# Kernel tuning notes

Measured on AMD Instinct MI355X. Metric: run time of the kernel, lower is better.

Reference implementation:

```python
import jax, jax.numpy as jnp
import numpy as np

N_NODES = 100000
N_EDGES = 3200000
IN_C, HID_C, OUT_C = 64, 128, 64


def gcn_conv(x, src, dst, W, b, n):
    """PyG GCNConv: h = x @ W; out[d] += norm(e) * h[s]; norm = deg^-1/2[s]*deg^-1/2[d].
    src/dst already include self-loops."""
    h = x @ W  # [N, out_c]
    deg = jax.ops.segment_sum(jnp.ones_like(dst, dtype=h.dtype), dst, num_segments=n)
    dinv = jnp.where(deg > 0, jax.lax.rsqrt(deg), 0.0)
    norm = dinv[src] * dinv[dst]  # [E]
    msg = h[src] * norm[:, None]  # [E, out_c] -- dominant memory traffic
    return jax.ops.segment_sum(msg, dst, num_segments=n) + b


def setup_inputs() -> dict:
    key = jax.random.key(0)
    k1, k2, k3, k4 = jax.random.split(key, 4)
    x = jax.random.normal(k1, (N_NODES, IN_C), dtype=jnp.float32)
    edge_index = jax.random.randint(k2, (2, N_EDGES), 0, N_NODES, dtype=jnp.int64)
    W1 = jax.random.normal(k3, (IN_C, HID_C), dtype=jnp.float32) / np.sqrt(IN_C)
    b1 = jnp.zeros((HID_C,), dtype=jnp.float32)
    W2 = jax.random.normal(k4, (HID_C, OUT_C), dtype=jnp.float32) / np.sqrt(HID_C)
    b2 = jnp.zeros((OUT_C,), dtype=jnp.float32)
    return {"x": x, "edge_index": edge_index, "W1": W1, "b1": b1, "W2": W2, "b2": b2}


def reference(x, edge_index, W1, b1, W2, b2):
    n = x.shape[0]
    loops = jnp.arange(n, dtype=edge_index.dtype)  # self-loops, as PyG GCNConv adds
    src = jnp.concatenate([edge_index[0], loops])
    dst = jnp.concatenate([edge_index[1], loops])
    h = gcn_conv(x, src, dst, W1, b1, n)
    h = jax.nn.relu(h)
    out = gcn_conv(h, src, dst, W2, b2, n)
    return out
```

## Files before the change

kernel.cpp:

```cpp
#include <hip/hip_runtime.h>
#include <math.h>


#define IN_C 64
#define HID_C 128
#define OUT_C 64
#define BSHIFT 9
#define BW (1 << BSHIFT)
#define NPB 512
#define CAP 24576
#define CH_MAX 6272

typedef __attribute__((ext_vector_type(8))) short bf16x8;
typedef __attribute__((ext_vector_type(4))) float f32x4;
typedef __attribute__((ext_vector_type(2))) float v2f;

__device__ __forceinline__ unsigned short f2bf(float f) {
  unsigned u = __float_as_uint(f);
  return (unsigned short)((u + 0x7FFF + ((u >> 16) & 1)) >> 16);
}
__device__ __forceinline__ v2f cvt2(unsigned u) {
  v2f r;
  r.x = __uint_as_float(u << 16);
  r.y = __uint_as_float(u & 0xFFFF0000u);
  return r;
}
__device__ __forceinline__ unsigned pack2(v2f v) {
  return ((unsigned)f2bf(v.y) << 16) | f2bf(v.x);
}


__global__ __launch_bounds__(256) void k_build(const int* __restrict__ ei, int e, int n,
    int nb, int* __restrict__ gcnt, unsigned* __restrict__ ebuf,
    const float* __restrict__ W1, const float* __restrict__ W2,
    unsigned short* __restrict__ Wt1, unsigned short* __restrict__ Wt2,
    unsigned short* __restrict__ xs_zero, unsigned short* __restrict__ h2s_zero) {
  const int t = threadIdx.x;
  if (blockIdx.x >= NPB) {
    int bb = blockIdx.x - NPB;
    if (bb == 32) {
      if (t < 64) { xs_zero[t] = 0; h2s_zero[t] = 0; }
      return;
    }
    int i = bb * 256 + t;
    if (i < IN_C * HID_C) {
      int k = i >> 7, c = i & (HID_C - 1);
      Wt1[c * IN_C + k] = f2bf(W1[i]);
    }
    if (i < HID_C * OUT_C) {
      int k = i >> 6, c = i & (OUT_C - 1);
      Wt2[c * HID_C + k] = f2bf(W2[i]);
    }
    return;
  }
  __shared__ unsigned lpay[CH_MAX];
  __shared__ unsigned char lbuck[CH_MAX];
  __shared__ int lh[256];
  __shared__ int lbase[256];
  __shared__ int lcur[256];
  __shared__ int sflag;
  if (t == 0) sflag = 0;
  __syncthreads();
  const int chunk = (e + NPB - 1) / NPB;
  const int lo = blockIdx.x * chunk;
  const int hi = min(lo + chunk, e);
  {
    int lim = min(hi, lo + 512);
    int f = 0;
    for (int i = lo + t; i < lim; i += 256)
      if (ei[2 * i + 1] != 0) f = 1;
    if (f) sflag = 1;
  }
  __syncthreads();
  const int f = sflag;
  for (int sub = lo; sub < hi; sub += CH_MAX) {
    const int shi = min(sub + CH_MAX, hi);
    const int mm = shi - sub;
    for (int i = t; i < nb; i += 256) lh[i] = 0;
    __syncthreads();
    for (int i = sub + t; i < shi; i += 256) {
      int s, d;
      if (f) {
        s = __builtin_nontemporal_load(&ei[i]);
        d = __builtin_nontemporal_load(&ei[e + i]);
      } else {
        s = (int)__builtin_nontemporal_load(&((const long long*)ei)[i]);
        d = (int)__builtin_nontemporal_load(&((const long long*)ei)[e + i]);
      }
      s = min(max(s, 0), n - 1);
      d = min(max(d, 0), n - 1);
      int bk = d >> BSHIFT;
      lpay[i - sub] = ((unsigned)(d & (BW - 1)) << 23) | (unsigned)s;
      lbuck[i - sub] = (unsigned char)bk;
      atomicAdd(&lh[bk], 1);
    }
    __syncthreads();
    for (int i = t; i < nb; i += 256) {
      int c = lh[i];
      lbase[i] = c ? atomicAdd(&gcnt[i], c) : 0;
      lcur[i] = 0;
    }
    __syncthreads();
    for (int i = t; i < mm; i += 256) {
      int bk = lbuck[i];
      int slot = lbase[bk] + atomicAdd(&lcur[bk], 1);
      if (slot < CAP) ebuf[(size_t)bk * CAP + slot] = lpay[i];
    }
    __syncthreads();
  }
}


__global__ __launch_bounds__(1024) void k_finalize(const unsigned* __restrict__ ebuf,
    const int* __restrict__ gcnt, const float* __restrict__ x,
    unsigned short* __restrict__ xs, int n, int nb,
    int* __restrict__ row_ptr, float* __restrict__ dinv, int* __restrict__ col) {
  __shared__ int sc[256];
  __shared__ int ldeg[BW];
  __shared__ int lofs[BW];
  __shared__ int lcur[BW];
  __shared__ float sdv[BW];
  __shared__ int wsum[256];
  const int b = blockIdx.x;
  const int t = threadIdx.x;
  const int T = 1024;
  int cnt = 0, nodes = 0;
  if (t < nb) {
    cnt = min(gcnt[t], CAP);
    nodes = min(BW, n - t * BW);
  }
  if (t < 256) sc[t] = cnt + nodes;
  __syncthreads();
  for (int off = 1; off < 256; off <<= 1) {
    int vc = 0;
    if (t < 256 && t >= off) vc = sc[t - off];
    __syncthreads();
    if (t < 256) sc[t] += vc;
    __syncthreads();
  }
  const int cntb = min(gcnt[b], CAP);
  const int eb = b * CAP;
  const int ee = eb + cntb;
  const int cb = (b == 0) ? 0 : sc[b - 1];
  const int lo = b * BW;
  const int nn = min(BW, n - lo);
  for (int k = t; k < BW; k += T) ldeg[k] = 0;
  __syncthreads();
  for (int k = t; k < nn; k += T) ldeg[k] = 1;
  __syncthreads();
  for (int j = eb + t; j < ee; j += T) {
    int dl = (int)(ebuf[j] >> 23);
    atomicAdd(&ldeg[dl], 1);
  }
  __syncthreads();
  int p0 = 0, p1 = 0;
  if (t < 256) {
    p0 = ldeg[2 * t]; p1 = ldeg[2 * t + 1];
    wsum[t] = p0 + p1;
  }
  __syncthreads();
  for (int off = 1; off < 256; off <<= 1) {
    int v = 0;
    if (t < 256 && t >= off) v = wsum[t - off];
    __syncthreads();
    if (t < 256) wsum[t] += v;
    __syncthreads();
  }
  if (t < 256) {
    int pb = (t == 0) ? 0 : wsum[t - 1];
    lofs[2 * t] = pb;
    lofs[2 * t + 1] = pb + p0;
  }
  __syncthreads();
  for (int k = t; k < nn; k += T) {
    int base = cb + lofs[k];
    float dv = rsqrtf((float)ldeg[k]);
    row_ptr[lo + k] = base;
    dinv[lo + k] = dv;
    sdv[k] = dv;
    col[base] = lo + k;
    lcur[k] = lofs[k] + 1;
  }
  if (b == nb - 1 && t == 0) row_ptr[n] = sc[nb - 1];
  __syncthreads();
  for (int j = eb + t; j < ee; j += T) {
    unsigned pk = ebuf[j];
    int s = (int)(pk & 0x7FFFFF);
    int dl = (int)(pk >> 23);
    int p = atomicAdd(&lcur[dl], 1);
    col[cb + p] = s;
  }
  const float4* x4 = (const float4*)x;
  for (int idx = t; idx < nn * 16; idx += T) {
    int row = idx >> 4, q = idx & 15;
    float sc2 = sdv[row];
    float4 v = x4[(size_t)(lo + row) * 16 + q];
    ushort4 o;
    o.x = f2bf(v.x * sc2); o.y = f2bf(v.y * sc2);
    o.z = f2bf(v.z * sc2); o.w = f2bf(v.w * sc2);
    ((ushort4*)xs)[(size_t)(lo + row) * 16 + q] = o;
  }
}


template<bool BIAS, bool OUT_BF16>
__global__ __launch_bounds__(256) void k_agg(const unsigned short* __restrict__ feat,
    const int* __restrict__ row_ptr, const int* __restrict__ col,
    const float* __restrict__ dinv, const float* __restrict__ bias,
    void* __restrict__ outv, int n) {
  const int wid = threadIdx.x >> 6;
  const int lane = threadIdx.x & 63;
  const int es = lane >> 3;
  const int c8 = lane & 7;
  const int d = blockIdx.x * 4 + wid;
  if (d >= n) return;
  const int beg = row_ptr[d], end = row_ptr[d + 1];
  const uint4* f16 = (const uint4*)feat;
  const int rem = end - beg - es;
  const int c = (rem > 0) ? ((rem + 7) >> 3) : 0;
  const int last = end - 1;
  v2f a0 = {0.f, 0.f}, a1 = {0.f, 0.f}, a2 = {0.f, 0.f}, a3 = {0.f, 0.f};
  for (int g = 0; g < c; g += 4) {
    int j0 = beg + es + 8 * g;
    int i0 = col[j0];
    int i1 = col[min(j0 + 8, last)];
    int i2 = col[min(j0 + 16, last)];
    int i3 = col[min(j0 + 24, last)];
    if (g + 1 >= c) i1 = n;
    if (g + 2 >= c) i2 = n;
    if (g + 3 >= c) i3 = n;
    uint4 u0 = f16[(size_t)i0 * 8 + c8];
    uint4 u1 = f16[(size_t)i1 * 8 + c8];
    uint4 u2 = f16[(size_t)i2 * 8 + c8];
    uint4 u3 = f16[(size_t)i3 * 8 + c8];
    a0 += cvt2(u0.x) + cvt2(u1.x) + cvt2(u2.x) + cvt2(u3.x);
    a1 += cvt2(u0.y) + cvt2(u1.y) + cvt2(u2.y) + cvt2(u3.y);
    a2 += cvt2(u0.z) + cvt2(u1.z) + cvt2(u2.z) + cvt2(u3.z);
    a3 += cvt2(u0.w) + cvt2(u1.w) + cvt2(u2.w) + cvt2(u3.w);
  }
#pragma unroll
  for (int off = 8; off <= 32; off <<= 1) {
    v2f o0, o1, o2, o3;
    o0.x = __shfl_xor(a0.x, off); o0.y = __shfl_xor(a0.y, off);
    o1.x = __shfl_xor(a1.x, off); o1.y = __shfl_xor(a1.y, off);
    o2.x = __shfl_xor(a2.x, off); o2.y = __shfl_xor(a2.y, off);
    o3.x = __shfl_xor(a3.x, off); o3.y = __shfl_xor(a3.y, off);
    a0 += o0; a1 += o1; a2 += o2; a3 += o3;
  }
  if (es == 0) {
    float sc = dinv[d];
    v2f vs = {sc, sc};
    a0 *= vs; a1 *= vs; a2 *= vs; a3 *= vs;
    if (BIAS) {
      const v2f* b2v = (const v2f*)bias;
      a0 += b2v[c8 * 4 + 0]; a1 += b2v[c8 * 4 + 1];
      a2 += b2v[c8 * 4 + 2]; a3 += b2v[c8 * 4 + 3];
    }
    if (OUT_BF16) {
      uint4 o;
      o.x = pack2(a0); o.y = pack2(a1); o.z = pack2(a2); o.w = pack2(a3);
      ((uint4*)outv)[(size_t)d * 8 + c8] = o;
    } else {
      float4* o4 = (float4*)outv;
      o4[(size_t)d * 16 + c8 * 2]     = make_float4(a0.x, a0.y, a1.x, a1.y);
      o4[(size_t)d * 16 + c8 * 2 + 1] = make_float4(a2.x, a2.y, a3.x, a3.y);
    }
  }
}


__global__ __launch_bounds__(256) void k_mlp(const unsigned short* __restrict__ A1,
    const unsigned short* __restrict__ Wt1, const unsigned short* __restrict__ Wt2,
    const float* __restrict__ b1, const float* __restrict__ dinv,
    unsigned short* __restrict__ h2s, int M) {
  __shared__ unsigned short sA[16 * 136];
  const int wv = threadIdx.x >> 6;
  const int lane = threadIdx.x & 63;
  const int m = lane & 15;
  const int q = lane >> 4;
  bf16x8 w1a[2], w1b[2], w2[4];
#pragma unroll
  for (int kt = 0; kt < 2; kt++) {
    w1a[kt] = *(const bf16x8*)&Wt1[(size_t)(wv * 16 + m) * IN_C + kt * 32 + q * 8];
    w1b[kt] = *(const bf16x8*)&Wt1[(size_t)((wv + 4) * 16 + m) * IN_C + kt * 32 + q * 8];
  }
#pragma unroll
  for (int kt = 0; kt < 4; kt++)
    w2[kt] = *(const bf16x8*)&Wt2[(size_t)(wv * 16 + m) * HID_C + kt * 32 + q * 8];
  const float bv0 = b1[wv * 16 + m];
  const float bv1 = b1[(wv + 4) * 16 + m];
  const int ntiles = (M + 15) >> 4;
  for (int tile = blockIdx.x; tile < ntiles; tile += gridDim.x) {
    const int r0 = tile * 16;
    const int ra = min(r0 + m, M - 1);
    f32x4 acc0 = {0.f, 0.f, 0.f, 0.f}, acc1 = {0.f, 0.f, 0.f, 0.f};
#pragma unroll
    for (int kt = 0; kt < 2; kt++) {
      bf16x8 a = *(const bf16x8*)&A1[(size_t)ra * IN_C + kt * 32 + q * 8];
      acc0 = __builtin_amdgcn_mfma_f32_16x16x32_bf16(a, w1a[kt], acc0, 0, 0, 0);
      acc1 = __builtin_amdgcn_mfma_f32_16x16x32_bf16(a, w1b[kt], acc1, 0, 0, 0);
    }
    float dv[4];
#pragma unroll
    for (int i = 0; i < 4; i++) dv[i] = dinv[min(r0 + q * 4 + i, M - 1)];
    {
      int c = wv * 16 + m;
#pragma unroll
      for (int i = 0; i < 4; i++)
        sA[(q * 4 + i) * 136 + c] = f2bf(fmaxf(acc0[i] + bv0, 0.f) * dv[i]);
      c = (wv + 4) * 16 + m;
#pragma unroll
      for (int i = 0; i < 4; i++)
        sA[(q * 4 + i) * 136 + c] = f2bf(fmaxf(acc1[i] + bv1, 0.f) * dv[i]);
    }
    __syncthreads();
    f32x4 acc = {0.f, 0.f, 0.f, 0.f};
#pragma unroll
    for (int kt = 0; kt < 4; kt++) {
      bf16x8 a = *(const bf16x8*)&sA[m * 136 + kt * 32 + q * 8];
      acc = __builtin_amdgcn_mfma_f32_16x16x32_bf16(a, w2[kt], acc, 0, 0, 0);
    }
    int c = wv * 16 + m;
#pragma unroll
    for (int i = 0; i < 4; i++) {
      int row = r0 + q * 4 + i;
      if (row < M) h2s[(size_t)row * OUT_C + c] = f2bf(acc[i]);
    }
    __syncthreads();
  }
}


extern "C" void kernel_launch(void* const* d_in, const int* in_sizes, int n_in,
                              void* d_out, int out_size, void* d_ws, size_t ws_size,
                              hipStream_t stream) {
  const float* x  = (const float*)d_in[0];
  const int*   ei = (const int*)d_in[1];
  const float* W1 = (const float*)d_in[2];
  const float* b1 = (const float*)d_in[3];
  const float* W2 = (const float*)d_in[4];
  const float* b2 = (const float*)d_in[5];
  float* out = (float*)d_out;

  const int n = in_sizes[0] / IN_C;
  const int e = in_sizes[1] / 2;
  const int nb = (n + BW - 1) >> BSHIFT;

  char* p = (char*)d_ws;
  auto alloc = [&](size_t bytes) {
    char* r = p;
    p += (bytes + 255) & ~(size_t)255;
    return r;
  };
  int*   gcnt       = (int*)alloc((size_t)nb * 4);
  int*   row_ptr    = (int*)alloc((size_t)(n + 1) * 4);
  float* dinv       = (float*)alloc((size_t)n * 4);
  int*   col        = (int*)alloc((size_t)(e + n) * 4);
  unsigned* ebuf    = (unsigned*)alloc((size_t)nb * CAP * 4);
  unsigned short* xs  = (unsigned short*)alloc((size_t)(n + 1) * IN_C * 2);
  unsigned short* A1  = (unsigned short*)alloc((size_t)n * IN_C * 2);
  unsigned short* h2s = (unsigned short*)alloc((size_t)(n + 1) * OUT_C * 2);
  unsigned short* Wt1 = (unsigned short*)alloc((size_t)IN_C * HID_C * 2);
  unsigned short* Wt2 = (unsigned short*)alloc((size_t)HID_C * OUT_C * 2);

  hipMemsetAsync(gcnt, 0, (size_t)nb * 4, stream);

  k_build<<<NPB + 33, 256, 0, stream>>>(ei, e, n, nb, gcnt, ebuf, W1, W2, Wt1, Wt2,
      xs + (size_t)n * IN_C, h2s + (size_t)n * OUT_C);
  k_finalize<<<nb, 1024, 0, stream>>>(ebuf, gcnt, x, xs, n, nb, row_ptr, dinv, col);

  k_agg<false, true><<<(n + 3) / 4, 256, 0, stream>>>(xs, row_ptr, col, dinv, nullptr, A1, n);
  k_mlp<<<1024, 256, 0, stream>>>(A1, Wt1, Wt2, b1, dinv, h2s, n);
  k_agg<true, false><<<(n + 3) / 4, 256, 0, stream>>>(h2s, row_ptr, col, dinv, b2, out, n);
}
```

Baseline: 279.6 us.

## Store layer-1 features column-chunked so each aggregation block gathers one 16-byte slice

Changes the scaled bf16 input features and the first aggregation output to a chunk-major layout of 8 column groups of 8 bf16 each. The first-layer aggregation becomes a new kernel in which each block handles one column group, with each wave covering 8 destination rows and 8 edge lanes per row. This is meant to shrink the gathered working set per pass, so each 1.6 MB slice fits in cache and random gathers hit L2 more often. In exchange the edge list and index reads are repeated 8 times, and the MLP reads A1 with a strided chunk-major access.

```diff
diff --git a/kernel.cpp b/kernel.cpp
--- a/kernel.cpp
+++ b/kernel.cpp
@@ -34,12 +34,16 @@
     int nb, int* __restrict__ gcnt, unsigned* __restrict__ ebuf,
     const float* __restrict__ W1, const float* __restrict__ W2,
     unsigned short* __restrict__ Wt1, unsigned short* __restrict__ Wt2,
-    unsigned short* __restrict__ xs_zero, unsigned short* __restrict__ h2s_zero) {
+    unsigned short* __restrict__ xs_cm, unsigned short* __restrict__ h2s_zero) {
   const int t = threadIdx.x;
   if (blockIdx.x >= NPB) {
     int bb = blockIdx.x - NPB;
     if (bb == 32) {
-      if (t < 64) { xs_zero[t] = 0; h2s_zero[t] = 0; }
+      if (t < 64) {
+        int c = t >> 3, k = t & 7;
+        xs_cm[((size_t)c * (n + 1) + n) * 8 + k] = 0;
+        h2s_zero[t] = 0;
+      }
       return;
     }
     int i = bb * 256 + t;
@@ -113,7 +117,7 @@
 
 __global__ __launch_bounds__(1024) void k_finalize(const unsigned* __restrict__ ebuf,
     const int* __restrict__ gcnt, const float* __restrict__ x,
-    unsigned short* __restrict__ xs, int n, int nb,
+    unsigned short* __restrict__ xs_cm, int n, int nb,
     int* __restrict__ row_ptr, float* __restrict__ dinv, int* __restrict__ col) {
   __shared__ int sc[256];
   __shared__ int ldeg[BW];
@@ -191,23 +195,83 @@
     col[cb + p] = s;
   }
   const float4* x4 = (const float4*)x;
-  for (int idx = t; idx < nn * 16; idx += T) {
-    int row = idx >> 4, q = idx & 15;
-    float sc2 = sdv[row];
-    float4 v = x4[(size_t)(lo + row) * 16 + q];
-    ushort4 o;
-    o.x = f2bf(v.x * sc2); o.y = f2bf(v.y * sc2);
-    o.z = f2bf(v.z * sc2); o.w = f2bf(v.w * sc2);
-    ((ushort4*)xs)[(size_t)(lo + row) * 16 + q] = o;
-  }
-}
-
-
-template<bool BIAS, bool OUT_BF16>
-__global__ __launch_bounds__(256) void k_agg(const unsigned short* __restrict__ feat,
+  uint4* xso = (uint4*)xs_cm;
+  for (int idx = t; idx < 8 * 512; idx += T) {
+    int c = idx >> 9, row = idx & 511;
+    if (row < nn) {
+      float sc2 = sdv[row];
+      float4 v0 = x4[(size_t)(lo + row) * 16 + c * 2];
+      float4 v1 = x4[(size_t)(lo + row) * 16 + c * 2 + 1];
+      uint4 o;
+      o.x = pack2(v2f{v0.x * sc2, v0.y * sc2});
+      o.y = pack2(v2f{v0.z * sc2, v0.w * sc2});
+      o.z = pack2(v2f{v1.x * sc2, v1.y * sc2});
+      o.w = pack2(v2f{v1.z * sc2, v1.w * sc2});
+      xso[(size_t)c * (n + 1) + lo + row] = o;
+    }
+  }
+}
+
+
+__global__ __launch_bounds__(256) void k_agg1c(const unsigned short* __restrict__ xs_cm,
+    const int* __restrict__ row_ptr, const int* __restrict__ col,
+    const float* __restrict__ dinv, unsigned short* __restrict__ A1_cm, int n) {
+  const int g = blockIdx.x & 7;
+  const int tile = blockIdx.x >> 3;
+  const int wv = threadIdx.x >> 6;
+  const int lane = threadIdx.x & 63;
+  const int rloc = lane >> 3;
+  const int es = lane & 7;
+  const int d = tile * 32 + wv * 8 + rloc;
+  if (d >= n) return;
+  const uint4* f = (const uint4*)xs_cm + (size_t)g * (n + 1);
+  const int beg = row_ptr[d], end = row_ptr[d + 1];
+  const int rem = end - beg - es;
+  const int c = (rem > 0) ? ((rem + 7) >> 3) : 0;
+  const int last = end - 1;
+  v2f a0 = {0.f, 0.f}, a1 = {0.f, 0.f}, a2 = {0.f, 0.f}, a3 = {0.f, 0.f};
+  for (int gi = 0; gi < c; gi += 4) {
+    int j0 = beg + es + 8 * gi;
+    int i0 = col[j0];
+    int i1 = col[min(j0 + 8, last)];
+    int i2 = col[min(j0 + 16, last)];
+    int i3 = col[min(j0 + 24, last)];
+    if (gi + 1 >= c) i1 = n;
+    if (gi + 2 >= c) i2 = n;
+    if (gi + 3 >= c) i3 = n;
+    uint4 u0 = f[i0];
+    uint4 u1 = f[i1];
+    uint4 u2 = f[i2];
+    uint4 u3 = f[i3];
+    a0 += cvt2(u0.x) + cvt2(u1.x) + cvt2(u2.x) + cvt2(u3.x);
+    a1 += cvt2(u0.y) + cvt2(u1.y) + cvt2(u2.y) + cvt2(u3.y);
+    a2 += cvt2(u0.z) + cvt2(u1.z) + cvt2(u2.z) + cvt2(u3.z);
+    a3 += cvt2(u0.w) + cvt2(u1.w) + cvt2(u2.w) + cvt2(u3.w);
+  }
+#pragma unroll
+  for (int off = 1; off <= 4; off <<= 1) {
+    v2f o0, o1, o2, o3;
+    o0.x = __shfl_xor(a0.x, off); o0.y = __shfl_xor(a0.y, off);
+    o1.x = __shfl_xor(a1.x, off); o1.y = __shfl_xor(a1.y, off);
+    o2.x = __shfl_xor(a2.x, off); o2.y = __shfl_xor(a2.y, off);
+    o3.x = __shfl_xor(a3.x, off); o3.y = __shfl_xor(a3.y, off);
+    a0 += o0; a1 += o1; a2 += o2; a3 += o3;
+  }
+  if (es == 0) {
+    float sc = dinv[d];
+    v2f vs = {sc, sc};
+    a0 *= vs; a1 *= vs; a2 *= vs; a3 *= vs;
+    uint4 o;
+    o.x = pack2(a0); o.y = pack2(a1); o.z = pack2(a2); o.w = pack2(a3);
+    ((uint4*)A1_cm)[(size_t)g * n + d] = o;
+  }
+}
+
+
+__global__ __launch_bounds__(256) void k_agg2(const unsigned short* __restrict__ feat,
     const int* __restrict__ row_ptr, const int* __restrict__ col,
     const float* __restrict__ dinv, const float* __restrict__ bias,
-    void* __restrict__ outv, int n) {
+    float* __restrict__ out, int n) {
   const int wid = threadIdx.x >> 6;
   const int lane = threadIdx.x & 63;
   const int es = lane >> 3;
@@ -251,25 +315,17 @@
     float sc = dinv[d];
     v2f vs = {sc, sc};
     a0 *= vs; a1 *= vs; a2 *= vs; a3 *= vs;
-    if (BIAS) {
-      const v2f* b2v = (const v2f*)bias;
-      a0 += b2v[c8 * 4 + 0]; a1 += b2v[c8 * 4 + 1];
-      a2 += b2v[c8 * 4 + 2]; a3 += b2v[c8 * 4 + 3];
-    }
-    if (OUT_BF16) {
-      uint4 o;
-      o.x = pack2(a0); o.y = pack2(a1); o.z = pack2(a2); o.w = pack2(a3);
-      ((uint4*)outv)[(size_t)d * 8 + c8] = o;
-    } else {
-      float4* o4 = (float4*)outv;
-      o4[(size_t)d * 16 + c8 * 2]     = make_float4(a0.x, a0.y, a1.x, a1.y);
-      o4[(size_t)d * 16 + c8 * 2 + 1] = make_float4(a2.x, a2.y, a3.x, a3.y);
-    }
-  }
-}
-
-
-__global__ __launch_bounds__(256) void k_mlp(const unsigned short* __restrict__ A1,
+    const v2f* b2v = (const v2f*)bias;
+    a0 += b2v[c8 * 4 + 0]; a1 += b2v[c8 * 4 + 1];
+    a2 += b2v[c8 * 4 + 2]; a3 += b2v[c8 * 4 + 3];
+    float4* o4 = (float4*)out;
+    o4[(size_t)d * 16 + c8 * 2]     = make_float4(a0.x, a0.y, a1.x, a1.y);
+    o4[(size_t)d * 16 + c8 * 2 + 1] = make_float4(a2.x, a2.y, a3.x, a3.y);
+  }
+}
+
+
+__global__ __launch_bounds__(256) void k_mlp(const unsigned short* __restrict__ A1_cm,
     const unsigned short* __restrict__ Wt1, const unsigned short* __restrict__ Wt2,
     const float* __restrict__ b1, const float* __restrict__ dinv,
     unsigned short* __restrict__ h2s, int M) {
@@ -296,7 +352,7 @@
     f32x4 acc0 = {0.f, 0.f, 0.f, 0.f}, acc1 = {0.f, 0.f, 0.f, 0.f};
 #pragma unroll
     for (int kt = 0; kt < 2; kt++) {
-      bf16x8 a = *(const bf16x8*)&A1[(size_t)ra * IN_C + kt * 32 + q * 8];
+      bf16x8 a = *(const bf16x8*)&A1_cm[((size_t)(kt * 4 + q) * M + ra) * 8];
       acc0 = __builtin_amdgcn_mfma_f32_16x16x32_bf16(a, w1a[kt], acc0, 0, 0, 0);
       acc1 = __builtin_amdgcn_mfma_f32_16x16x32_bf16(a, w1b[kt], acc1, 0, 0, 0);
     }
@@ -357,8 +413,8 @@
   float* dinv       = (float*)alloc((size_t)n * 4);
   int*   col        = (int*)alloc((size_t)(e + n) * 4);
   unsigned* ebuf    = (unsigned*)alloc((size_t)nb * CAP * 4);
-  unsigned short* xs  = (unsigned short*)alloc((size_t)(n + 1) * IN_C * 2);
-  unsigned short* A1  = (unsigned short*)alloc((size_t)n * IN_C * 2);
+  unsigned short* xs_cm = (unsigned short*)alloc((size_t)8 * (n + 1) * 8 * 2);
+  unsigned short* A1_cm = (unsigned short*)alloc((size_t)8 * n * 8 * 2);
   unsigned short* h2s = (unsigned short*)alloc((size_t)(n + 1) * OUT_C * 2);
   unsigned short* Wt1 = (unsigned short*)alloc((size_t)IN_C * HID_C * 2);
   unsigned short* Wt2 = (unsigned short*)alloc((size_t)HID_C * OUT_C * 2);
@@ -366,10 +422,10 @@
   hipMemsetAsync(gcnt, 0, (size_t)nb * 4, stream);
 
   k_build<<<NPB + 33, 256, 0, stream>>>(ei, e, n, nb, gcnt, ebuf, W1, W2, Wt1, Wt2,
-      xs + (size_t)n * IN_C, h2s + (size_t)n * OUT_C);
-  k_finalize<<<nb, 1024, 0, stream>>>(ebuf, gcnt, x, xs, n, nb, row_ptr, dinv, col);
-
-  k_agg<false, true><<<(n + 3) / 4, 256, 0, stream>>>(xs, row_ptr, col, dinv, nullptr, A1, n);
-  k_mlp<<<1024, 256, 0, stream>>>(A1, Wt1, Wt2, b1, dinv, h2s, n);
-  k_agg<true, false><<<(n + 3) / 4, 256, 0, stream>>>(h2s, row_ptr, col, dinv, b2, out, n);
-}
+      xs_cm, h2s + (size_t)n * OUT_C);
+  k_finalize<<<nb, 1024, 0, stream>>>(ebuf, gcnt, x, xs_cm, n, nb, row_ptr, dinv, col);
+
+  k_agg1c<<<8 * ((n + 31) / 32), 256, 0, stream>>>(xs_cm, row_ptr, col, dinv, A1_cm, n);
+  k_mlp<<<1024, 256, 0, stream>>>(A1_cm, Wt1, Wt2, b1, dinv, h2s, n);
+  k_agg2<<<(n + 3) / 4, 256, 0, stream>>>(h2s, row_ptr, col, dinv, b2, out, n);
+}
```

After: 344.1 us. 1.23x slower.

## Fuse first-layer aggregation with the dense MLP into one persistent kernel

Applied to the files above, without the earlier changes.

Merges the first sparse aggregation and the two-matmul MLP into a single persistent kernel. Each block gathers 16 destination rows into shared memory, then runs the MFMA transforms on them directly, so the intermediate A1 buffer is no longer written to or read back from global memory and one launch disappears. In exchange, the gather phase now runs in a persistent grid of 2048 blocks that hold MLP weights in registers. That may reduce occupancy and latency hiding for the memory-bound gather, and adds block-wide barriers per tile.

```diff
diff --git a/kernel.cpp b/kernel.cpp
--- a/kernel.cpp
+++ b/kernel.cpp
@@ -203,11 +203,125 @@
 }
 
 
-template<bool BIAS, bool OUT_BF16>
-__global__ __launch_bounds__(256) void k_agg(const unsigned short* __restrict__ feat,
+__global__ __launch_bounds__(256) void k_aggmlp(const unsigned short* __restrict__ feat,
+    const int* __restrict__ row_ptr, const int* __restrict__ col,
+    const float* __restrict__ dinv, const unsigned short* __restrict__ Wt1,
+    const unsigned short* __restrict__ Wt2, const float* __restrict__ b1,
+    unsigned short* __restrict__ h2s, int n) {
+  __shared__ __align__(16) unsigned short sA1[16][72];
+  __shared__ __align__(16) unsigned short sH[16][136];
+  const int wv = threadIdx.x >> 6;
+  const int lane = threadIdx.x & 63;
+  const int es = lane >> 3;
+  const int c8 = lane & 7;
+  const int m = lane & 15;
+  const int q = lane >> 4;
+  const uint4* f16 = (const uint4*)feat;
+  bf16x8 w1a[2], w1b[2], w2[4];
+#pragma unroll
+  for (int kt = 0; kt < 2; kt++) {
+    w1a[kt] = *(const bf16x8*)&Wt1[(size_t)(wv * 16 + m) * IN_C + kt * 32 + q * 8];
+    w1b[kt] = *(const bf16x8*)&Wt1[(size_t)((wv + 4) * 16 + m) * IN_C + kt * 32 + q * 8];
+  }
+#pragma unroll
+  for (int kt = 0; kt < 4; kt++)
+    w2[kt] = *(const bf16x8*)&Wt2[(size_t)(wv * 16 + m) * HID_C + kt * 32 + q * 8];
+  const float bv0 = b1[wv * 16 + m];
+  const float bv1 = b1[(wv + 4) * 16 + m];
+  const int ntiles = (n + 15) >> 4;
+  for (int tile = blockIdx.x; tile < ntiles; tile += gridDim.x) {
+    const int r0 = tile * 16;
+    for (int rr = 0; rr < 4; ++rr) {
+      const int d = r0 + wv * 4 + rr;
+      if (d < n) {
+        const int beg = row_ptr[d], end = row_ptr[d + 1];
+        const int rem = end - beg - es;
+        const int c = (rem > 0) ? ((rem + 7) >> 3) : 0;
+        const int last = end - 1;
+        v2f a0 = {0.f, 0.f}, a1 = {0.f, 0.f}, a2 = {0.f, 0.f}, a3 = {0.f, 0.f};
+        for (int g = 0; g < c; g += 4) {
+          int j0 = beg + es + 8 * g;
+          int i0 = col[j0];
+          int i1 = col[min(j0 + 8, last)];
+          int i2 = col[min(j0 + 16, last)];
+          int i3 = col[min(j0 + 24, last)];
+          if (g + 1 >= c) i1 = n;
+          if (g + 2 >= c) i2 = n;
+          if (g + 3 >= c) i3 = n;
+          uint4 u0 = f16[(size_t)i0 * 8 + c8];
+          uint4 u1 = f16[(size_t)i1 * 8 + c8];
+          uint4 u2 = f16[(size_t)i2 * 8 + c8];
+          uint4 u3 = f16[(size_t)i3 * 8 + c8];
+          a0 += cvt2(u0.x) + cvt2(u1.x) + cvt2(u2.x) + cvt2(u3.x);
+          a1 += cvt2(u0.y) + cvt2(u1.y) + cvt2(u2.y) + cvt2(u3.y);
+          a2 += cvt2(u0.z) + cvt2(u1.z) + cvt2(u2.z) + cvt2(u3.z);
+          a3 += cvt2(u0.w) + cvt2(u1.w) + cvt2(u2.w) + cvt2(u3.w);
+        }
+#pragma unroll
+        for (int off = 8; off <= 32; off <<= 1) {
+          v2f o0, o1, o2, o3;
+          o0.x = __shfl_xor(a0.x, off); o0.y = __shfl_xor(a0.y, off);
+          o1.x = __shfl_xor(a1.x, off); o1.y = __shfl_xor(a1.y, off);
+          o2.x = __shfl_xor(a2.x, off); o2.y = __shfl_xor(a2.y, off);
+          o3.x = __shfl_xor(a3.x, off); o3.y = __shfl_xor(a3.y, off);
+          a0 += o0; a1 += o1; a2 += o2; a3 += o3;
+        }
+        if (es == 0) {
+          float sc = dinv[d];
+          v2f vs = {sc, sc};
+          a0 *= vs; a1 *= vs; a2 *= vs; a3 *= vs;
+          uint4 o;
+          o.x = pack2(a0); o.y = pack2(a1); o.z = pack2(a2); o.w = pack2(a3);
+          *(uint4*)&sA1[wv * 4 + rr][c8 * 8] = o;
+        }
+      } else if (es == 0) {
+        uint4 z = {0u, 0u, 0u, 0u};
+        *(uint4*)&sA1[wv * 4 + rr][c8 * 8] = z;
+      }
+    }
+    __syncthreads();
+    f32x4 acc0 = {0.f, 0.f, 0.f, 0.f}, acc1 = {0.f, 0.f, 0.f, 0.f};
+#pragma unroll
+    for (int kt = 0; kt < 2; kt++) {
+      bf16x8 a = *(const bf16x8*)&sA1[m][kt * 32 + q * 8];
+      acc0 = __builtin_amdgcn_mfma_f32_16x16x32_bf16(a, w1a[kt], acc0, 0, 0, 0);
+      acc1 = __builtin_amdgcn_mfma_f32_16x16x32_bf16(a, w1b[kt], acc1, 0, 0, 0);
+    }
+    float dv[4];
+#pragma unroll
+    for (int i = 0; i < 4; i++) dv[i] = dinv[min(r0 + q * 4 + i, n - 1)];
+    {
+      int c = wv * 16 + m;
+#pragma unroll
+      for (int i = 0; i < 4; i++)
+        sH[q * 4 + i][c] = f2bf(fmaxf(acc0[i] + bv0, 0.f) * dv[i]);
+      c = (wv + 4) * 16 + m;
+#pragma unroll
+      for (int i = 0; i < 4; i++)
+        sH[q * 4 + i][c] = f2bf(fmaxf(acc1[i] + bv1, 0.f) * dv[i]);
+    }
+    __syncthreads();
+    f32x4 acc = {0.f, 0.f, 0.f, 0.f};
+#pragma unroll
+    for (int kt = 0; kt < 4; kt++) {
+      bf16x8 a = *(const bf16x8*)&sH[m][kt * 32 + q * 8];
+      acc = __builtin_amdgcn_mfma_f32_16x16x32_bf16(a, w2[kt], acc, 0, 0, 0);
+    }
+    int c = wv * 16 + m;
+#pragma unroll
+    for (int i = 0; i < 4; i++) {
+      int row = r0 + q * 4 + i;
+      if (row < n) h2s[(size_t)row * OUT_C + c] = f2bf(acc[i]);
+    }
+    __syncthreads();
+  }
+}
+
+
+__global__ __launch_bounds__(256) void k_agg2(const unsigned short* __restrict__ feat,
     const int* __restrict__ row_ptr, const int* __restrict__ col,
     const float* __restrict__ dinv, const float* __restrict__ bias,
-    void* __restrict__ outv, int n) {
+    float* __restrict__ out, int n) {
   const int wid = threadIdx.x >> 6;
   const int lane = threadIdx.x & 63;
   const int es = lane >> 3;
@@ -251,82 +365,12 @@
     float sc = dinv[d];
     v2f vs = {sc, sc};
     a0 *= vs; a1 *= vs; a2 *= vs; a3 *= vs;
-    if (BIAS) {
-      const v2f* b2v = (const v2f*)bias;
-      a0 += b2v[c8 * 4 + 0]; a1 += b2v[c8 * 4 + 1];
-      a2 += b2v[c8 * 4 + 2]; a3 += b2v[c8 * 4 + 3];
-    }
-    if (OUT_BF16) {
-      uint4 o;
-      o.x = pack2(a0); o.y = pack2(a1); o.z = pack2(a2); o.w = pack2(a3);
-      ((uint4*)outv)[(size_t)d * 8 + c8] = o;
-    } else {
-      float4* o4 = (float4*)outv;
-      o4[(size_t)d * 16 + c8 * 2]     = make_float4(a0.x, a0.y, a1.x, a1.y);
-      o4[(size_t)d * 16 + c8 * 2 + 1] = make_float4(a2.x, a2.y, a3.x, a3.y);
-    }
-  }
-}
-
-
-__global__ __launch_bounds__(256) void k_mlp(const unsigned short* __restrict__ A1,
-    const unsigned short* __restrict__ Wt1, const unsigned short* __restrict__ Wt2,
-    const float* __restrict__ b1, const float* __restrict__ dinv,
-    unsigned short* __restrict__ h2s, int M) {
-  __shared__ unsigned short sA[16 * 136];
-  const int wv = threadIdx.x >> 6;
-  const int lane = threadIdx.x & 63;
-  const int m = lane & 15;
-  const int q = lane >> 4;
-  bf16x8 w1a[2], w1b[2], w2[4];
-#pragma unroll
-  for (int kt = 0; kt < 2; kt++) {
-    w1a[kt] = *(const bf16x8*)&Wt1[(size_t)(wv * 16 + m) * IN_C + kt * 32 + q * 8];
-    w1b[kt] = *(const bf16x8*)&Wt1[(size_t)((wv + 4) * 16 + m) * IN_C + kt * 32 + q * 8];
-  }
-#pragma unroll
-  for (int kt = 0; kt < 4; kt++)
-    w2[kt] = *(const bf16x8*)&Wt2[(size_t)(wv * 16 + m) * HID_C + kt * 32 + q * 8];
-  const float bv0 = b1[wv * 16 + m];
-  const float bv1 = b1[(wv + 4) * 16 + m];
-  const int ntiles = (M + 15) >> 4;
-  for (int tile = blockIdx.x; tile < ntiles; tile += gridDim.x) {
-    const int r0 = tile * 16;
-    const int ra = min(r0 + m, M - 1);
-    f32x4 acc0 = {0.f, 0.f, 0.f, 0.f}, acc1 = {0.f, 0.f, 0.f, 0.f};
-#pragma unroll
-    for (int kt = 0; kt < 2; kt++) {
-      bf16x8 a = *(const bf16x8*)&A1[(size_t)ra * IN_C + kt * 32 + q * 8];
-      acc0 = __builtin_amdgcn_mfma_f32_16x16x32_bf16(a, w1a[kt], acc0, 0, 0, 0);
-      acc1 = __builtin_amdgcn_mfma_f32_16x16x32_bf16(a, w1b[kt], acc1, 0, 0, 0);
-    }
-    float dv[4];
-#pragma unroll
-    for (int i = 0; i < 4; i++) dv[i] = dinv[min(r0 + q * 4 + i, M - 1)];
-    {
-      int c = wv * 16 + m;
-#pragma unroll
-      for (int i = 0; i < 4; i++)
-        sA[(q * 4 + i) * 136 + c] = f2bf(fmaxf(acc0[i] + bv0, 0.f) * dv[i]);
-      c = (wv + 4) * 16 + m;
-#pragma unroll
-      for (int i = 0; i < 4; i++)
-        sA[(q * 4 + i) * 136 + c] = f2bf(fmaxf(acc1[i] + bv1, 0.f) * dv[i]);
-    }
-    __syncthreads();
-    f32x4 acc = {0.f, 0.f, 0.f, 0.f};
-#pragma unroll
-    for (int kt = 0; kt < 4; kt++) {
-      bf16x8 a = *(const bf16x8*)&sA[m * 136 + kt * 32 + q * 8];
-      acc = __builtin_amdgcn_mfma_f32_16x16x32_bf16(a, w2[kt], acc, 0, 0, 0);
-    }
-    int c = wv * 16 + m;
-#pragma unroll
-    for (int i = 0; i < 4; i++) {
-      int row = r0 + q * 4 + i;
-      if (row < M) h2s[(size_t)row * OUT_C + c] = f2bf(acc[i]);
-    }
-    __syncthreads();
+    const v2f* b2v = (const v2f*)bias;
+    a0 += b2v[c8 * 4 + 0]; a1 += b2v[c8 * 4 + 1];
+    a2 += b2v[c8 * 4 + 2]; a3 += b2v[c8 * 4 + 3];
+    float4* o4 = (float4*)out;
+    o4[(size_t)d * 16 + c8 * 2]     = make_float4(a0.x, a0.y, a1.x, a1.y);
+    o4[(size_t)d * 16 + c8 * 2 + 1] = make_float4(a2.x, a2.y, a3.x, a3.y);
   }
 }
 
@@ -358,7 +402,6 @@
   int*   col        = (int*)alloc((size_t)(e + n) * 4);
   unsigned* ebuf    = (unsigned*)alloc((size_t)nb * CAP * 4);
   unsigned short* xs  = (unsigned short*)alloc((size_t)(n + 1) * IN_C * 2);
-  unsigned short* A1  = (unsigned short*)alloc((size_t)n * IN_C * 2);
   unsigned short* h2s = (unsigned short*)alloc((size_t)(n + 1) * OUT_C * 2);
   unsigned short* Wt1 = (unsigned short*)alloc((size_t)IN_C * HID_C * 2);
   unsigned short* Wt2 = (unsigned short*)alloc((size_t)HID_C * OUT_C * 2);
@@ -369,7 +412,6 @@
       xs + (size_t)n * IN_C, h2s + (size_t)n * OUT_C);
   k_finalize<<<nb, 1024, 0, stream>>>(ebuf, gcnt, x, xs, n, nb, row_ptr, dinv, col);
 
-  k_agg<false, true><<<(n + 3) / 4, 256, 0, stream>>>(xs, row_ptr, col, dinv, nullptr, A1, n);
-  k_mlp<<<1024, 256, 0, stream>>>(A1, Wt1, Wt2, b1, dinv, h2s, n);
-  k_agg<true, false><<<(n + 3) / 4, 256, 0, stream>>>(h2s, row_ptr, col, dinv, b2, out, n);
-}
+  k_aggmlp<<<2048, 256, 0, stream>>>(xs, row_ptr, col, dinv, Wt1, Wt2, b1, h2s, n);
+  k_agg2<<<(n + 3) / 4, 256, 0, stream>>>(h2s, row_ptr, col, dinv, b2, out, n);
+}
```

Measured after the change: 294.0 us. 5.2% more time.
